# Kernel tuning notes

Hardware: AMD Instinct MI355X
Metric: run time of the kernel (lower is better)

Reference implementation:

```python
import jax, jax.numpy as jnp
import numpy as np

N_NODES = 50000
N_EDGES = 1600000
IN_DIM = 128
OUT_DIM = 64
HEADS = 4
NEG_SLOPE = 0.2


def setup_inputs() -> dict:
    key = jax.random.key(0)
    ks = jax.random.split(key, 6)
    x = jax.random.normal(ks[0], (N_NODES, IN_DIM), dtype=jnp.float32)
    edge_index = jax.random.randint(ks[1], (2, N_EDGES), 0, N_NODES, dtype=jnp.int64)
    scale = 1.0 / np.sqrt(IN_DIM)
    W = jax.random.normal(ks[2], (IN_DIM, HEADS * OUT_DIM), dtype=jnp.float32) * scale
    att_src = jax.random.normal(ks[3], (HEADS, OUT_DIM), dtype=jnp.float32) * scale
    att_dst = jax.random.normal(ks[4], (HEADS, OUT_DIM), dtype=jnp.float32) * scale
    bias = jnp.zeros((HEADS * OUT_DIM,), dtype=jnp.float32)
    return {"x": x, "edge_index": edge_index, "W": W, "att_src": att_src, "att_dst": att_dst, "bias": bias}


def reference(x, edge_index, W, att_src, att_dst, bias):
    N = x.shape[0]
    H, F = att_src.shape
    # PyG GATConv default: add self-loops (static shape: E + N edges)
    loops = jnp.arange(N, dtype=edge_index.dtype)
    ei = jnp.concatenate([edge_index, jnp.stack([loops, loops])], axis=1)
    src, dst = ei[0], ei[1]
    # linear projection, split heads: [N, H, F]
    h = (x @ W).reshape(N, H, F)
    # per-node attention logits per head: [N, H]
    a_s = jnp.einsum('nhf,hf->nh', h, att_src)
    a_d = jnp.einsum('nhf,hf->nh', h, att_dst)
    # per-edge score: gather + LeakyReLU -> [E, H]
    e = jax.nn.leaky_relu(a_s[src] + a_d[dst], negative_slope=NEG_SLOPE)
    # segment softmax over incoming edges of each dst node
    m = jax.ops.segment_max(e, dst, num_segments=N)
    ex = jnp.exp(e - m[dst])
    s = jax.ops.segment_sum(ex, dst, num_segments=N)
    alpha = ex / (s[dst] + 1e-16)
    # weighted message scatter-aggregate: [N, H, F]
    msg = h[src] * alpha[:, :, None]
    out = jax.ops.segment_sum(msg, dst, num_segments=N)
    return out.reshape(N, H * F) + bias
```

## Files before the change

### kernel.cpp

```cpp
#include <hip/hip_runtime.h>

constexpr int N_NODES = 50000;
constexpr int N_EDGES = 1600000;
constexpr int E_TOT   = N_EDGES + N_NODES;
constexpr int IN_DIM  = 128;
constexpr int HEADS   = 4;
constexpr int FDIM    = 64;
constexpr int HF      = 256;
constexpr float NEG   = 0.2f;
constexpr int NB_SCAN = (N_NODES + 255) / 256;
constexpr int NPX     = (N_NODES + 7) / 8;
constexpr int FILL_CH = 16384;
constexpr int FILL_K  = (E_TOT + FILL_CH - 1) / FILL_CH;

__device__ __forceinline__ float leaky(float t) {
    return fmaxf(t, 0.f) + NEG * fminf(t, 0.f);
}

__device__ __forceinline__ unsigned short f2bf(float f) {
    unsigned int u = __float_as_uint(f);
    u += 0x7fffu + ((u >> 16) & 1u);
    return (unsigned short)(u >> 16);
}
__device__ __forceinline__ float bf_lo(unsigned int u) {
    return __uint_as_float(u << 16);
}
__device__ __forceinline__ float bf_hi(unsigned int u) {
    return __uint_as_float(u & 0xffff0000u);
}

__device__ __forceinline__ int wave_incl_scan(int v, int lane) {
    #pragma unroll
    for (int off = 1; off < 64; off <<= 1) {
        int n = __shfl_up(v, off);
        if (lane >= off) v += n;
    }
    return v;
}

__global__ __launch_bounds__(256) void gemm_kernel(const float* __restrict__ x,
                                                   const float* __restrict__ W,
                                                   const float* __restrict__ att_src,
                                                   const float* __restrict__ att_dst,
                                                   unsigned short* __restrict__ h_bf,
                                                   float* __restrict__ a_s,
                                                   float* __restrict__ a_d) {
    __shared__ float xs[IN_DIM][64];
    const int t = threadIdx.x;
    const int node0 = blockIdx.x * 64;

    {
        const int r  = t & 63;
        const int k0 = (t >> 6) * 32;
        int row = node0 + r;
        if (row >= N_NODES) row = N_NODES - 1;
        const float4* src = reinterpret_cast<const float4*>(&x[row * IN_DIM + k0]);
        #pragma unroll
        for (int i = 0; i < 8; ++i) {
            float4 v = src[i];
            int k = k0 + i * 4;
            xs[k + 0][r] = v.x;
            xs[k + 1][r] = v.y;
            xs[k + 2][r] = v.z;
            xs[k + 3][r] = v.w;
        }
    }
    __syncthreads();

    const int l  = t & 63;
    const int c  = l * 4;
    const int rg = (t >> 6) * 16;
    float acc[16][4];
    #pragma unroll
    for (int r = 0; r < 16; ++r)
        #pragma unroll
        for (int j = 0; j < 4; ++j) acc[r][j] = 0.f;

    #pragma unroll 2
    for (int k = 0; k < IN_DIM; ++k) {
        const float4 wv = *reinterpret_cast<const float4*>(&W[k * HF + c]);
        const float4 xa = *reinterpret_cast<const float4*>(&xs[k][rg + 0]);
        const float4 xb = *reinterpret_cast<const float4*>(&xs[k][rg + 4]);
        const float4 xc = *reinterpret_cast<const float4*>(&xs[k][rg + 8]);
        const float4 xd = *reinterpret_cast<const float4*>(&xs[k][rg + 12]);
        const float xr[16] = {xa.x, xa.y, xa.z, xa.w, xb.x, xb.y, xb.z, xb.w,
                              xc.x, xc.y, xc.z, xc.w, xd.x, xd.y, xd.z, xd.w};
        #pragma unroll
        for (int r = 0; r < 16; ++r) {
            acc[r][0] = fmaf(xr[r], wv.x, acc[r][0]);
            acc[r][1] = fmaf(xr[r], wv.y, acc[r][1]);
            acc[r][2] = fmaf(xr[r], wv.z, acc[r][2]);
            acc[r][3] = fmaf(xr[r], wv.w, acc[r][3]);
        }
    }

    const float4 asv = *reinterpret_cast<const float4*>(&att_src[c]);
    const float4 adv = *reinterpret_cast<const float4*>(&att_dst[c]);
    #pragma unroll
    for (int r = 0; r < 16; ++r) {
        float ps = acc[r][0] * asv.x + acc[r][1] * asv.y +
                   acc[r][2] * asv.z + acc[r][3] * asv.w;
        float pd = acc[r][0] * adv.x + acc[r][1] * adv.y +
                   acc[r][2] * adv.z + acc[r][3] * adv.w;
        #pragma unroll
        for (int off = 1; off < 16; off <<= 1) {
            ps += __shfl_xor(ps, off);
            pd += __shfl_xor(pd, off);
        }
        const int node = node0 + rg + r;
        if ((l & 15) == 0 && node < N_NODES) {
            a_s[node * HEADS + (l >> 4)] = ps;
            a_d[node * HEADS + (l >> 4)] = pd;
        }
    }

    #pragma unroll
    for (int r = 0; r < 16; ++r) {
        const int node = node0 + rg + r;
        if (node < N_NODES) {
            ushort4 v;
            v.x = f2bf(acc[r][0]); v.y = f2bf(acc[r][1]);
            v.z = f2bf(acc[r][2]); v.w = f2bf(acc[r][3]);
            *reinterpret_cast<ushort4*>(&h_bf[node * HF + c]) = v;
        }
    }
}

__global__ void zero_kernel(int* __restrict__ counts) {
    const int i = blockIdx.x * blockDim.x + threadIdx.x;
    if (i < N_NODES) counts[i] = 0;
}

__global__ void hist_kernel(const int* __restrict__ ei,
                            int* __restrict__ counts,
                            int* __restrict__ rank) {
    const int e = blockIdx.x * blockDim.x + threadIdx.x;
    if (e >= E_TOT) return;
    const int dst = (e < N_EDGES) ? ei[N_EDGES + e] : e - N_EDGES;
    rank[e] = atomicAdd(&counts[dst], 1);
}

__global__ __launch_bounds__(256) void scanA_kernel(const int* __restrict__ counts,
                                                    int* __restrict__ local,
                                                    int* __restrict__ bsum) {
    const int t = threadIdx.x, lane = t & 63, w = t >> 6;
    const int i = blockIdx.x * 256 + t;
    const int v = (i < N_NODES) ? counts[i] : 0;
    const int inc = wave_incl_scan(v, lane);
    __shared__ int wt[4];
    if (lane == 63) wt[w] = inc;
    __syncthreads();
    int base = 0;
    #pragma unroll
    for (int k = 0; k < 3; ++k) if (k < w) base += wt[k];
    if (i < N_NODES) local[i] = base + inc - v;
    if (t == 255) bsum[blockIdx.x] = base + inc;
}

__global__ __launch_bounds__(256) void scanB_kernel(const int* __restrict__ bsum,
                                                    int* __restrict__ boff) {
    const int t = threadIdx.x, lane = t & 63, w = t >> 6;
    const int v = (t < NB_SCAN) ? bsum[t] : 0;
    const int inc = wave_incl_scan(v, lane);
    __shared__ int wt[4];
    if (lane == 63) wt[w] = inc;
    __syncthreads();
    int base = 0;
    #pragma unroll
    for (int k = 0; k < 3; ++k) if (k < w) base += wt[k];
    if (t < NB_SCAN) boff[t] = base + inc - v;
}

__global__ __launch_bounds__(256) void scanC_kernel(const int* __restrict__ local,
                                                    const int* __restrict__ boff,
                                                    int* __restrict__ offsets) {
    const int i = blockIdx.x * 256 + threadIdx.x;
    if (i < N_NODES) offsets[i] = local[i] + boff[blockIdx.x];
    if (i == 0) offsets[N_NODES] = E_TOT;
}

__global__ __launch_bounds__(256) void fill_kernel(const int* __restrict__ ei,
                                                   const int* __restrict__ rank,
                                                   const int* __restrict__ offsets,
                                                   int* __restrict__ sorted_src) {
    const int bid = blockIdx.x;
    const int lo  = (bid & 7) * NPX;
    const int hi  = min(N_NODES, lo + NPX);
    const int e0  = (bid >> 3) * FILL_CH;
    const int e1  = min(E_TOT, e0 + FILL_CH);
    for (int e = e0 + threadIdx.x; e < e1; e += 256) {
        const int dst = (e < N_EDGES) ? ei[N_EDGES + e] : e - N_EDGES;
        if (dst >= lo && dst < hi) {
            const int src = (e < N_EDGES) ? ei[e] : dst;
            sorted_src[offsets[dst] + rank[e]] = src;
        }
    }
}

__global__ __launch_bounds__(256) void gather_kernel(const int* __restrict__ sorted_src,
                                                     const float* __restrict__ a_s,
                                                     const float* __restrict__ a_d,
                                                     const int* __restrict__ offsets,
                                                     const unsigned short* __restrict__ h_bf,
                                                     const float* __restrict__ bias,
                                                     float* __restrict__ out) {
    const int dst  = (blockIdx.x * 256 + threadIdx.x) >> 6;
    const int lane = threadIdx.x & 63;
    if (dst >= N_NODES) return;
    const int half = lane >> 5;
    const int il   = lane & 31;
    const int hd   = il >> 3;

    const int beg = __builtin_amdgcn_readfirstlane(offsets[dst]);
    const int end = __builtin_amdgcn_readfirstlane(offsets[dst + 1]);
    const float ad = a_d[dst * HEADS + hd];

    float a0 = 0.f, a1 = 0.f, a2 = 0.f, a3 = 0.f;
    float a4 = 0.f, a5 = 0.f, a6 = 0.f, a7 = 0.f;
    float dsum = 0.f;

    auto body = [&](int slot) {
        const int   src = sorted_src[slot];
        const float as  = a_s[src * HEADS + hd];
        const float ex  = expf(leaky(as + ad));
        const uint4 hv  = *reinterpret_cast<const uint4*>(&h_bf[src * HF + il * 8]);
        a0 = fmaf(ex, bf_lo(hv.x), a0); a1 = fmaf(ex, bf_hi(hv.x), a1);
        a2 = fmaf(ex, bf_lo(hv.y), a2); a3 = fmaf(ex, bf_hi(hv.y), a3);
        a4 = fmaf(ex, bf_lo(hv.z), a4); a5 = fmaf(ex, bf_hi(hv.z), a5);
        a6 = fmaf(ex, bf_lo(hv.w), a6); a7 = fmaf(ex, bf_hi(hv.w), a7);
        dsum += ex;
    };

    int j = beg;
    for (; j + 7 < end; j += 8) {
        body(j + half);
        body(j + 2 + half);
        body(j + 4 + half);
        body(j + 6 + half);
    }
    for (; j + 1 < end; j += 2) body(j + half);
    if (j < end && half == 0) body(j);

    a0 += __shfl_xor(a0, 32); a1 += __shfl_xor(a1, 32);
    a2 += __shfl_xor(a2, 32); a3 += __shfl_xor(a3, 32);
    a4 += __shfl_xor(a4, 32); a5 += __shfl_xor(a5, 32);
    a6 += __shfl_xor(a6, 32); a7 += __shfl_xor(a7, 32);
    dsum += __shfl_xor(dsum, 32);

    const float inv = 1.f / (dsum + 1e-16f);
    const int eo = il * 8 + half * 4;
    const float4 bv = *reinterpret_cast<const float4*>(&bias[eo]);
    float4 o;
    o.x = (half ? a4 : a0) * inv + bv.x;
    o.y = (half ? a5 : a1) * inv + bv.y;
    o.z = (half ? a6 : a2) * inv + bv.z;
    o.w = (half ? a7 : a3) * inv + bv.w;
    *reinterpret_cast<float4*>(&out[dst * HF + eo]) = o;
}

extern "C" void kernel_launch(void* const* d_in, const int* in_sizes, int n_in,
                              void* d_out, int out_size, void* d_ws, size_t ws_size,
                              hipStream_t stream) {
    const float* x       = (const float*)d_in[0];
    const int*   ei      = (const int*)d_in[1];
    const float* W       = (const float*)d_in[2];
    const float* att_src = (const float*)d_in[3];
    const float* att_dst = (const float*)d_in[4];
    const float* bias    = (const float*)d_in[5];
    float* out = (float*)d_out;

    char* ws = (char*)d_ws;
    unsigned short* h_bf = (unsigned short*)(ws);
    float*  a_s        = (float*) (ws + 25600000);
    float*  a_d        = (float*) (ws + 26400000);
    int*    counts     = (int*)   (ws + 27200000);
    int*    offsets    = (int*)   (ws + 27400000);
    int*    rank       = (int*)   (ws + 27600016);
    int*    sorted_src = (int*)   (ws + 34200016);
    int*    local      = (int*)   (ws + 40800016);
    int*    bsum       = (int*)   (ws + 41000016);
    int*    boff       = (int*)   (ws + 41000800);

    gemm_kernel<<<(N_NODES + 63) / 64, 256, 0, stream>>>(x, W, att_src, att_dst,
                                                         h_bf, a_s, a_d);
    zero_kernel<<<(N_NODES + 255) / 256, 256, 0, stream>>>(counts);
    hist_kernel<<<(E_TOT + 255) / 256, 256, 0, stream>>>(ei, counts, rank);
    scanA_kernel<<<NB_SCAN, 256, 0, stream>>>(counts, local, bsum);
    scanB_kernel<<<1, 256, 0, stream>>>(bsum, boff);
    scanC_kernel<<<NB_SCAN, 256, 0, stream>>>(local, boff, offsets);
    fill_kernel<<<8 * FILL_K, 256, 0, stream>>>(ei, rank, offsets, sorted_src);
    const long total_threads = (long)N_NODES * 64;
    gather_kernel<<<(int)((total_threads + 255) / 256), 256, 0, stream>>>(
        sorted_src, a_s, a_d, offsets, h_bf, bias, out);
}
```

Measured before the change: 392.9 us.

## Fuse CSR build kernels into one cooperative kernel with grid syncs

New measurement: 1.159 ms. 195% more time.

```diff
diff --git a/kernel.cpp b/kernel.cpp
--- a/kernel.cpp
+++ b/kernel.cpp
@@ -1,4 +1,7 @@
 #include <hip/hip_runtime.h>
+#include <hip/hip_cooperative_groups.h>
+
+namespace cg = cooperative_groups;
 
 constexpr int N_NODES = 50000;
 constexpr int N_EDGES = 1600000;
@@ -12,6 +15,7 @@
 constexpr int NPX     = (N_NODES + 7) / 8;
 constexpr int FILL_CH = 16384;
 constexpr int FILL_K  = (E_TOT + FILL_CH - 1) / FILL_CH;
+constexpr int COOP_B  = 1024;
 
 __device__ __forceinline__ float leaky(float t) {
     return fmaxf(t, 0.f) + NEG * fminf(t, 0.f);
@@ -126,73 +130,79 @@
     }
 }
 
-__global__ void zero_kernel(int* __restrict__ counts) {
-    const int i = blockIdx.x * blockDim.x + threadIdx.x;
-    if (i < N_NODES) counts[i] = 0;
-}
-
-__global__ void hist_kernel(const int* __restrict__ ei,
-                            int* __restrict__ counts,
-                            int* __restrict__ rank) {
-    const int e = blockIdx.x * blockDim.x + threadIdx.x;
-    if (e >= E_TOT) return;
-    const int dst = (e < N_EDGES) ? ei[N_EDGES + e] : e - N_EDGES;
-    rank[e] = atomicAdd(&counts[dst], 1);
-}
-
-__global__ __launch_bounds__(256) void scanA_kernel(const int* __restrict__ counts,
-                                                    int* __restrict__ local,
-                                                    int* __restrict__ bsum) {
-    const int t = threadIdx.x, lane = t & 63, w = t >> 6;
-    const int i = blockIdx.x * 256 + t;
-    const int v = (i < N_NODES) ? counts[i] : 0;
-    const int inc = wave_incl_scan(v, lane);
+__global__ __launch_bounds__(256, 4) void sort_kernel(const int* __restrict__ ei,
+                                                      int* __restrict__ counts,
+                                                      int* __restrict__ rank,
+                                                      int* __restrict__ local,
+                                                      int* __restrict__ bsum,
+                                                      int* __restrict__ boff,
+                                                      int* __restrict__ offsets,
+                                                      int* __restrict__ sorted_src) {
+    cg::grid_group grid = cg::this_grid();
     __shared__ int wt[4];
-    if (lane == 63) wt[w] = inc;
-    __syncthreads();
-    int base = 0;
-    #pragma unroll
-    for (int k = 0; k < 3; ++k) if (k < w) base += wt[k];
-    if (i < N_NODES) local[i] = base + inc - v;
-    if (t == 255) bsum[blockIdx.x] = base + inc;
-}
-
-__global__ __launch_bounds__(256) void scanB_kernel(const int* __restrict__ bsum,
-                                                    int* __restrict__ boff) {
-    const int t = threadIdx.x, lane = t & 63, w = t >> 6;
-    const int v = (t < NB_SCAN) ? bsum[t] : 0;
-    const int inc = wave_incl_scan(v, lane);
-    __shared__ int wt[4];
-    if (lane == 63) wt[w] = inc;
-    __syncthreads();
-    int base = 0;
-    #pragma unroll
-    for (int k = 0; k < 3; ++k) if (k < w) base += wt[k];
-    if (t < NB_SCAN) boff[t] = base + inc - v;
-}
-
-__global__ __launch_bounds__(256) void scanC_kernel(const int* __restrict__ local,
-                                                    const int* __restrict__ boff,
-                                                    int* __restrict__ offsets) {
-    const int i = blockIdx.x * 256 + threadIdx.x;
-    if (i < N_NODES) offsets[i] = local[i] + boff[blockIdx.x];
-    if (i == 0) offsets[N_NODES] = E_TOT;
-}
-
-__global__ __launch_bounds__(256) void fill_kernel(const int* __restrict__ ei,
-                                                   const int* __restrict__ rank,
-                                                   const int* __restrict__ offsets,
-                                                   int* __restrict__ sorted_src) {
-    const int bid = blockIdx.x;
-    const int lo  = (bid & 7) * NPX;
-    const int hi  = min(N_NODES, lo + NPX);
-    const int e0  = (bid >> 3) * FILL_CH;
-    const int e1  = min(E_TOT, e0 + FILL_CH);
-    for (int e = e0 + threadIdx.x; e < e1; e += 256) {
+    const int tid = blockIdx.x * 256 + threadIdx.x;
+    const int nth = COOP_B * 256;
+
+    for (int i = tid; i < N_NODES; i += nth) counts[i] = 0;
+    __threadfence();
+    grid.sync();
+
+    for (int e = tid; e < E_TOT; e += nth) {
         const int dst = (e < N_EDGES) ? ei[N_EDGES + e] : e - N_EDGES;
-        if (dst >= lo && dst < hi) {
-            const int src = (e < N_EDGES) ? ei[e] : dst;
-            sorted_src[offsets[dst] + rank[e]] = src;
+        rank[e] = atomicAdd(&counts[dst], 1);
+    }
+    __threadfence();
+    grid.sync();
+
+    if (blockIdx.x < NB_SCAN) {
+        const int t = threadIdx.x, lane = t & 63, w = t >> 6;
+        const int i = blockIdx.x * 256 + t;
+        const int v = (i < N_NODES) ? counts[i] : 0;
+        const int inc = wave_incl_scan(v, lane);
+        if (lane == 63) wt[w] = inc;
+        __syncthreads();
+        int base = 0;
+        #pragma unroll
+        for (int k = 0; k < 3; ++k) if (k < w) base += wt[k];
+        if (i < N_NODES) local[i] = base + inc - v;
+        if (t == 255) bsum[blockIdx.x] = base + inc;
+    }
+    __threadfence();
+    grid.sync();
+
+    if (blockIdx.x == 0) {
+        const int t = threadIdx.x, lane = t & 63, w = t >> 6;
+        const int v = (t < NB_SCAN) ? bsum[t] : 0;
+        const int inc = wave_incl_scan(v, lane);
+        if (lane == 63) wt[w] = inc;
+        __syncthreads();
+        int base = 0;
+        #pragma unroll
+        for (int k = 0; k < 3; ++k) if (k < w) base += wt[k];
+        if (t < NB_SCAN) boff[t] = base + inc - v;
+    }
+    __threadfence();
+    grid.sync();
+
+    for (int i = tid; i < N_NODES; i += nth) offsets[i] = local[i] + boff[i >> 8];
+    if (tid == 0) offsets[N_NODES] = E_TOT;
+    __threadfence();
+    grid.sync();
+
+    {
+        const int xcd = blockIdx.x & 7;
+        const int lo  = xcd * NPX;
+        const int hi  = min(N_NODES, lo + NPX);
+        for (int sl = blockIdx.x >> 3; sl < FILL_K; sl += COOP_B >> 3) {
+            const int e0 = sl * FILL_CH;
+            const int e1 = min(E_TOT, e0 + FILL_CH);
+            for (int e = e0 + (int)threadIdx.x; e < e1; e += 256) {
+                const int dst = (e < N_EDGES) ? ei[N_EDGES + e] : e - N_EDGES;
+                if (dst >= lo && dst < hi) {
+                    const int src = (e < N_EDGES) ? ei[e] : dst;
+                    sorted_src[offsets[dst] + rank[e]] = src;
+                }
+            }
         }
     }
 }
@@ -222,7 +232,7 @@
     auto body = [&](int slot) {
         const int   src = sorted_src[slot];
         const float as  = a_s[src * HEADS + hd];
-        const float ex  = expf(leaky(as + ad));
+        const float ex  = __expf(leaky(as + ad));
         const uint4 hv  = *reinterpret_cast<const uint4*>(&h_bf[src * HF + il * 8]);
         a0 = fmaf(ex, bf_lo(hv.x), a0); a1 = fmaf(ex, bf_hi(hv.x), a1);
         a2 = fmaf(ex, bf_lo(hv.y), a2); a3 = fmaf(ex, bf_hi(hv.y), a3);
@@ -283,12 +293,12 @@
 
     gemm_kernel<<<(N_NODES + 63) / 64, 256, 0, stream>>>(x, W, att_src, att_dst,
                                                          h_bf, a_s, a_d);
-    zero_kernel<<<(N_NODES + 255) / 256, 256, 0, stream>>>(counts);
-    hist_kernel<<<(E_TOT + 255) / 256, 256, 0, stream>>>(ei, counts, rank);
-    scanA_kernel<<<NB_SCAN, 256, 0, stream>>>(counts, local, bsum);
-    scanB_kernel<<<1, 256, 0, stream>>>(bsum, boff);
-    scanC_kernel<<<NB_SCAN, 256, 0, stream>>>(local, boff, offsets);
-    fill_kernel<<<8 * FILL_K, 256, 0, stream>>>(ei, rank, offsets, sorted_src);
+
+    void* args[] = {(void*)&ei, (void*)&counts, (void*)&rank, (void*)&local,
+                    (void*)&bsum, (void*)&boff, (void*)&offsets, (void*)&sorted_src};
+    hipLaunchCooperativeKernel(reinterpret_cast<void*>(sort_kernel),
+                               dim3(COOP_B), dim3(256), args, 0, stream);
+
     const long total_threads = (long)N_NODES * 64;
     gather_kernel<<<(int)((total_threads + 255) / 256), 256, 0, stream>>>(
         sorted_src, a_s, a_d, offsets, h_bf, bias, out);
```
